# Kernel tuning notes

Measured on AMD Instinct MI355X. Metric: run time of the kernel, lower is better.

## Reference

```python
import jax, jax.numpy as jnp
import numpy as np

N = 100000          # nodes
E = 1600000         # edges (before self-loops)
F_IN = 128          # dataset.num_node_features
HID = 32            # hidden_channels
HEADS = 4
NUM_CLASSES = 40
NEG_SLOPE = 0.2     # PyG GATConv default


def setup_inputs() -> dict:
    key = jax.random.key(0)
    ks = jax.random.split(key, 16)
    x = jax.random.normal(ks[0], (N, F_IN), dtype=jnp.float32)
    edge_index = jax.random.randint(ks[1], (2, E), 0, N, dtype=jnp.int64)

    def glorot(k, shape):
        lim = float(np.sqrt(6.0 / (shape[0] + shape[-1])))
        return jax.random.uniform(k, shape, jnp.float32, -lim, lim)

    # layer 0: F_IN -> HID, heads=HEADS, concat
    W0 = glorot(ks[2], (F_IN, HEADS * HID))
    as0 = glorot(ks[3], (HEADS, HID))
    ad0 = glorot(ks[4], (HEADS, HID))
    b0 = jnp.zeros((HEADS * HID,), jnp.float32)
    # layer 1: HEADS*HID -> HID, heads=HEADS, concat
    W1 = glorot(ks[5], (HEADS * HID, HEADS * HID))
    as1 = glorot(ks[6], (HEADS, HID))
    ad1 = glorot(ks[7], (HEADS, HID))
    b1 = jnp.zeros((HEADS * HID,), jnp.float32)
    # layer 2: HEADS*HID -> HID, heads=1, no concat
    W2 = glorot(ks[8], (HEADS * HID, HID))
    as2 = glorot(ks[9], (1, HID))
    ad2 = glorot(ks[10], (1, HID))
    b2 = jnp.zeros((HID,), jnp.float32)
    # final linear HID -> NUM_CLASSES
    lin_w = glorot(ks[11], (HID, NUM_CLASSES))
    lin_b = jnp.zeros((NUM_CLASSES,), jnp.float32)
    return dict(x=x, edge_index=edge_index, W0=W0, as0=as0, ad0=ad0, b0=b0,
                W1=W1, as1=as1, ad1=ad1, b1=b1,
                W2=W2, as2=as2, ad2=ad2, b2=b2, lin_w=lin_w, lin_b=lin_b)


def gat_conv(x, src, dst, W, a_src, a_dst, b, heads, out_ch, concat):
    n = x.shape[0]
    h = (x @ W).reshape(n, heads, out_ch)               # [N,H,C]
    alpha_s = (h * a_src).sum(-1)                        # [N,H]
    alpha_d = (h * a_dst).sum(-1)                        # [N,H]
    e = jax.nn.leaky_relu(alpha_s[src] + alpha_d[dst], NEG_SLOPE)  # [E,H]
    m = jax.ops.segment_max(e, dst, num_segments=n)      # segment softmax over in-edges
    e = jnp.exp(e - m[dst])
    denom = jax.ops.segment_sum(e, dst, num_segments=n)
    alpha = e / (denom[dst] + 1e-16)                     # [E,H]
    out = jax.ops.segment_sum(h[src] * alpha[:, :, None], dst, num_segments=n)  # [N,H,C]
    out = out.reshape(n, heads * out_ch) if concat else out.mean(axis=1)
    return out + b


def reference(x, edge_index, W0, as0, ad0, b0, W1, as1, ad1, b1,
              W2, as2, ad2, b2, lin_w, lin_b):
    n = x.shape[0]
    loop = jnp.arange(n, dtype=edge_index.dtype)
    src = jnp.concatenate([edge_index[0], loop])   # PyG GATConv adds self-loops
    dst = jnp.concatenate([edge_index[1], loop])
    x = jax.nn.relu(gat_conv(x, src, dst, W0, as0, ad0, b0, HEADS, HID, True))
    x = jax.nn.relu(gat_conv(x, src, dst, W1, as1, ad1, b1, HEADS, HID, True))
    x = jax.nn.relu(gat_conv(x, src, dst, W2, as2, ad2, b2, 1, HID, False))
    return x @ lin_w + lin_b
```

## Files before the change

### kernel.cpp

```cpp
#include <hip/hip_runtime.h>
#include <hip/hip_bf16.h>
#include <hip/hip_fp16.h>
#include <math.h>


#define NEG_SLOPE 0.2f

typedef __attribute__((ext_vector_type(8))) _Float16 f16x8;
typedef __attribute__((ext_vector_type(4))) float    f32x4;


__global__ void zero1_kernel(int* __restrict__ a, int n) {
    int i = blockIdx.x * blockDim.x + threadIdx.x;
    if (i < n) a[i] = 0;
}

__global__ void count_rank_kernel(const int* __restrict__ ei, int eraw, int n,
                                  int* __restrict__ deg, int* __restrict__ rank) {
    int i = blockIdx.x * blockDim.x + threadIdx.x;
    int etot = eraw + n;
    if (i >= etot) return;
    int dst = (i < eraw) ? ei[eraw + i] : (i - eraw);
    rank[i] = atomicAdd(&deg[dst], 1);
}

__global__ __launch_bounds__(1024)
void scan_local_kernel(const int* __restrict__ deg, int* __restrict__ rowptr,
                       int* __restrict__ bsum, int n) {
    __shared__ int buf[1024];
    int tid = threadIdx.x;
    int i = blockIdx.x * 1024 + tid;
    int v = (i < n) ? deg[i] : 0;
    buf[tid] = v;
    __syncthreads();
    for (int off = 1; off < 1024; off <<= 1) {
        int t = (tid >= off) ? buf[tid - off] : 0;
        __syncthreads();
        buf[tid] += t;
        __syncthreads();
    }
    if (i < n) rowptr[i] = buf[tid] - v;
    if (tid == 1023) bsum[blockIdx.x] = buf[1023];
}

__global__ __launch_bounds__(128)
void scan_sums_kernel(const int* __restrict__ bsum, int* __restrict__ boffs, int nb) {
    __shared__ int buf[128];
    int tid = threadIdx.x;
    int v = (tid < nb) ? bsum[tid] : 0;
    buf[tid] = v;
    __syncthreads();
    for (int off = 1; off < 128; off <<= 1) {
        int t = (tid >= off) ? buf[tid - off] : 0;
        __syncthreads();
        buf[tid] += t;
        __syncthreads();
    }
    if (tid < nb) boffs[tid] = buf[tid] - v;
}

__global__ void scan_add_kernel(int* __restrict__ rowptr, const int* __restrict__ boffs,
                                int n, int etot) {
    int i = blockIdx.x * blockDim.x + threadIdx.x;
    if (i < n) rowptr[i] += boffs[i >> 10];
    if (i == 0) rowptr[n] = etot;
}

__global__ void scatter2_kernel(const int* __restrict__ ei, const int* __restrict__ rank,
                                int eraw, int n, const int* __restrict__ rowptr,
                                int* __restrict__ csr_src) {
    int i = blockIdx.x * blockDim.x + threadIdx.x;
    int etot = eraw + n;
    if (i >= etot) return;
    int src, dst;
    if (i < eraw) { src = ei[i]; dst = ei[eraw + i]; }
    else          { src = i - eraw; dst = src; }
    csr_src[rowptr[dst] + rank[i]] = src;
}


__global__ void wt_f16_kernel(const float* __restrict__ W, __half* __restrict__ Wt) {
    int i = blockIdx.x * blockDim.x + threadIdx.x;
    int k = i >> 7, c = i & 127;
    Wt[c * 128 + k] = __float2half(W[i]);
}


__global__ __launch_bounds__(256)
void gemm_mfma_f32in_kernel(const float* __restrict__ X, const __half* __restrict__ Wt,
                            __half* __restrict__ H, int n) {
    int t = threadIdx.x;
    int wave = t >> 6, lane = t & 63;
    int l15 = lane & 15;
    int kg  = lane >> 4;
    int base = blockIdx.x * 64 + wave * 16;
    int row  = base + l15;
    int rowc = (row < n) ? row : 0;

    f32x4 acc[8];
#pragma unroll
    for (int i = 0; i < 8; i++) acc[i] = (f32x4){0.f, 0.f, 0.f, 0.f};

    const float* xp = X + (size_t)rowc * 128 + kg * 8;
#pragma unroll
    for (int ks = 0; ks < 4; ks++) {
        float4 x0 = *(const float4*)(xp + ks * 32);
        float4 x1 = *(const float4*)(xp + ks * 32 + 4);
        f16x8 a;
        a[0] = (_Float16)x0.x; a[1] = (_Float16)x0.y; a[2] = (_Float16)x0.z; a[3] = (_Float16)x0.w;
        a[4] = (_Float16)x1.x; a[5] = (_Float16)x1.y; a[6] = (_Float16)x1.z; a[7] = (_Float16)x1.w;
#pragma unroll
        for (int ct = 0; ct < 8; ct++) {
            f16x8 b = *(const f16x8*)(Wt + (size_t)(ct * 16 + l15) * 128 + ks * 32 + kg * 8);
            acc[ct] = __builtin_amdgcn_mfma_f32_16x16x32_f16(a, b, acc[ct], 0, 0, 0);
        }
    }

#pragma unroll
    for (int ct = 0; ct < 8; ct++) {
#pragma unroll
        for (int r = 0; r < 4; r++) {
            int orow = base + kg * 4 + r;
            if (orow < n)
                H[(size_t)orow * 128 + ct * 16 + l15] = __float2half(acc[ct][r]);
        }
    }
}

__global__ __launch_bounds__(256)
void gemm_mfma_f16in_kernel(const __half* __restrict__ X, const __half* __restrict__ Wt,
                            __half* __restrict__ H, int n) {
    int t = threadIdx.x;
    int wave = t >> 6, lane = t & 63;
    int l15 = lane & 15;
    int kg  = lane >> 4;
    int base = blockIdx.x * 64 + wave * 16;
    int row  = base + l15;
    int rowc = (row < n) ? row : 0;

    f32x4 acc[8];
#pragma unroll
    for (int i = 0; i < 8; i++) acc[i] = (f32x4){0.f, 0.f, 0.f, 0.f};

    const __half* xp = X + (size_t)rowc * 128 + kg * 8;
#pragma unroll
    for (int ks = 0; ks < 4; ks++) {
        f16x8 a = *(const f16x8*)(xp + ks * 32);
#pragma unroll
        for (int ct = 0; ct < 8; ct++) {
            f16x8 b = *(const f16x8*)(Wt + (size_t)(ct * 16 + l15) * 128 + ks * 32 + kg * 8);
            acc[ct] = __builtin_amdgcn_mfma_f32_16x16x32_f16(a, b, acc[ct], 0, 0, 0);
        }
    }

#pragma unroll
    for (int ct = 0; ct < 8; ct++) {
#pragma unroll
        for (int r = 0; r < 4; r++) {
            int orow = base + kg * 4 + r;
            if (orow < n)
                H[(size_t)orow * 128 + ct * 16 + l15] = __float2half(acc[ct][r]);
        }
    }
}


__global__ __launch_bounds__(128)
void gemm_l2_f16_kernel(const __half* __restrict__ X, const float* __restrict__ W,
                        __half* __restrict__ H, int n) {
    __shared__ float xs[8][129];
    int base = blockIdx.x * 8;
    int tid = threadIdx.x;
#pragma unroll
    for (int it = 0; it < 4; it++) {
        int i = tid + it * 128;
        int r = i >> 6, c2 = i & 63;
        int row = base + r;
        __half2 v = (row < n) ? ((const __half2*)(X + (size_t)row * 128))[c2]
                              : __floats2half2_rn(0.f, 0.f);
        float2 f = __half22float2(v);
        xs[r][c2 * 2] = f.x; xs[r][c2 * 2 + 1] = f.y;
    }
    __syncthreads();
    int col  = tid & 31;
    int rsub = tid >> 5;
    float acc0 = 0.f, acc1 = 0.f;
    for (int k = 0; k < 128; k++) {
        float w = W[k * 32 + col];
        acc0 += xs[rsub][k] * w;
        acc1 += xs[rsub + 4][k] * w;
    }
    int row0 = base + rsub;
    if (row0 < n)     H[(size_t)row0 * 32 + col]       = __float2half(acc0);
    if (row0 + 4 < n) H[(size_t)(row0 + 4) * 32 + col] = __float2half(acc1);
}


__global__ void attn_coef_f16_kernel(const __half* __restrict__ H,
                                     const float* __restrict__ a_s,
                                     const float* __restrict__ a_d,
                                     float* __restrict__ as_out,
                                     float* __restrict__ ad_out, int n) {
    int i = blockIdx.x * blockDim.x + threadIdx.x;
    if (i >= n * 4) return;
    int node = i >> 2, h = i & 3;
    const __half2* hp = (const __half2*)(H + (size_t)node * 128 + h * 32);
    float s = 0.f, d = 0.f;
#pragma unroll
    for (int c2 = 0; c2 < 16; c2++) {
        float2 v = __half22float2(hp[c2]);
        s += v.x * a_s[h * 32 + c2 * 2] + v.y * a_s[h * 32 + c2 * 2 + 1];
        d += v.x * a_d[h * 32 + c2 * 2] + v.y * a_d[h * 32 + c2 * 2 + 1];
    }
    as_out[i] = s;
    ad_out[i] = d;
}

__global__ void attn_coef_l2_f16_kernel(const __half* __restrict__ H,
                                        const float* __restrict__ a_s,
                                        const float* __restrict__ a_d,
                                        float* __restrict__ as_out,
                                        float* __restrict__ ad_out, int n) {
    int i = blockIdx.x * blockDim.x + threadIdx.x;
    if (i >= n) return;
    const __half2* hp = (const __half2*)(H + (size_t)i * 32);
    float s = 0.f, d = 0.f;
#pragma unroll
    for (int c2 = 0; c2 < 16; c2++) {
        float2 v = __half22float2(hp[c2]);
        s += v.x * a_s[2 * c2] + v.y * a_s[2 * c2 + 1];
        d += v.x * a_d[2 * c2] + v.y * a_d[2 * c2 + 1];
    }
    as_out[i] = s;
    ad_out[i] = d;
}


struct h4pack { __half2 a, b; };

__global__ __launch_bounds__(256)
void gat_fused_f16_kernel(const __half* __restrict__ Hm,
                          const float* __restrict__ as_,
                          const float* __restrict__ ad_,
                          const int* __restrict__ rowptr,
                          const int* __restrict__ csr,
                          const float* __restrict__ bias,
                          __half* __restrict__ out, int n) {
    constexpr int GS = 32;
    int t = threadIdx.x;
    int node = blockIdx.x * 8 + (t >> 5);
    if (node >= n) return;
    int tl = t & 31;
    int h  = tl >> 3;
    int k8 = tl & 7;
    const uint2* H8 = (const uint2*)Hm;
    int e0 = rowptr[node], e1 = rowptr[node + 1];
    float ad_d = ad_[(size_t)node * 4 + h];

    int  ce  = e0 + k8;
    bool vA  = ce < e1;
    int  idxA = vA ? csr[ce] : 0;
    float asA = vA ? as_[(size_t)idxA * 4 + h] : 0.f;

    float m = -INFINITY, l = 0.f;
    float4 acc = make_float4(0.f, 0.f, 0.f, 0.f);

    for (int eb = e0; eb < e1; eb += 8) {
        uint2 u[8];
#pragma unroll
        for (int j = 0; j < 8; j++) {
            int src = __shfl(idxA, j, 8);
            u[j] = H8[(size_t)src * GS + tl];
        }

        int  ne  = eb + 8 + k8;
        bool vB  = ne < e1;
        int  idxB = vB ? csr[ne] : 0;
        float asB = vB ? as_[(size_t)idxB * 4 + h] : 0.f;

        float el = asA + ad_d;
        el = (el > 0.f) ? el : NEG_SLOPE * el;
        el = vA ? el : -INFINITY;

        float cm = el;
        cm = fmaxf(cm, __shfl_xor(cm, 1, 8));
        cm = fmaxf(cm, __shfl_xor(cm, 2, 8));
        cm = fmaxf(cm, __shfl_xor(cm, 4, 8));
        float m_new = fmaxf(m, cm);
        float scale = __expf(m - m_new);
        float p = vA ? __expf(el - m_new) : 0.f;

        float ps = p;
        ps += __shfl_xor(ps, 1, 8);
        ps += __shfl_xor(ps, 2, 8);
        ps += __shfl_xor(ps, 4, 8);
        l = l * scale + ps;
        acc.x *= scale; acc.y *= scale; acc.z *= scale; acc.w *= scale;
        m = m_new;

#pragma unroll
        for (int j = 0; j < 8; j++) {
            float pj  = __shfl(p, j, 8);
            float2 f01 = __half22float2(*(const __half2*)&u[j].x);
            float2 f23 = __half22float2(*(const __half2*)&u[j].y);
            acc.x += pj * f01.x; acc.y += pj * f01.y;
            acc.z += pj * f23.x; acc.w += pj * f23.y;
        }
        idxA = idxB; asA = asB; vA = vB;
    }

    float li = 1.f / (l + 1e-16f);
    float4 b4 = ((const float4*)bias)[tl];
    float4 o;
    o.x = fmaxf(acc.x * li + b4.x, 0.f);
    o.y = fmaxf(acc.y * li + b4.y, 0.f);
    o.z = fmaxf(acc.z * li + b4.z, 0.f);
    o.w = fmaxf(acc.w * li + b4.w, 0.f);
    h4pack po;
    po.a = __floats2half2_rn(o.x, o.y);
    po.b = __floats2half2_rn(o.z, o.w);
    ((h4pack*)out)[(size_t)node * 32 + tl] = po;
}


__global__ __launch_bounds__(256)
void gat_fused_l2_kernel(const __half* __restrict__ Hm,
                         const float* __restrict__ as_,
                         const float* __restrict__ ad_,
                         const int* __restrict__ rowptr,
                         const int* __restrict__ csr,
                         const float* __restrict__ bias,
                         const float* __restrict__ lw,
                         const float* __restrict__ lb,
                         float* __restrict__ out, int n) {
    int t = threadIdx.x;
    int node = blockIdx.x * 32 + (t >> 3);
    if (node >= n) return;
    int tl = t & 7;
    const uint2* H8 = (const uint2*)Hm;
    int e0 = rowptr[node], e1 = rowptr[node + 1];
    float ad_d = ad_[node];

    int  ce  = e0 + tl;
    bool vA  = ce < e1;
    int  idxA = vA ? csr[ce] : 0;
    float asA = vA ? as_[idxA] : 0.f;

    float m = -INFINITY, l = 0.f;
    float4 acc = make_float4(0.f, 0.f, 0.f, 0.f);

    for (int eb = e0; eb < e1; eb += 8) {
        uint2 u[8];
#pragma unroll
        for (int j = 0; j < 8; j++) {
            int src = __shfl(idxA, j, 8);
            u[j] = H8[(size_t)src * 8 + tl];
        }

        int  ne  = eb + 8 + tl;
        bool vB  = ne < e1;
        int  idxB = vB ? csr[ne] : 0;
        float asB = vB ? as_[idxB] : 0.f;

        float el = asA + ad_d;
        el = (el > 0.f) ? el : NEG_SLOPE * el;
        el = vA ? el : -INFINITY;

        float cm = el;
        cm = fmaxf(cm, __shfl_xor(cm, 1, 8));
        cm = fmaxf(cm, __shfl_xor(cm, 2, 8));
        cm = fmaxf(cm, __shfl_xor(cm, 4, 8));
        float m_new = fmaxf(m, cm);
        float scale = __expf(m - m_new);
        float p = vA ? __expf(el - m_new) : 0.f;

        float ps = p;
        ps += __shfl_xor(ps, 1, 8);
        ps += __shfl_xor(ps, 2, 8);
        ps += __shfl_xor(ps, 4, 8);
        l = l * scale + ps;
        acc.x *= scale; acc.y *= scale; acc.z *= scale; acc.w *= scale;
        m = m_new;

#pragma unroll
        for (int j = 0; j < 8; j++) {
            float pj  = __shfl(p, j, 8);
            float2 f01 = __half22float2(*(const __half2*)&u[j].x);
            float2 f23 = __half22float2(*(const __half2*)&u[j].y);
            acc.x += pj * f01.x; acc.y += pj * f01.y;
            acc.z += pj * f23.x; acc.w += pj * f23.y;
        }
        idxA = idxB; asA = asB; vA = vB;
    }

    float li = 1.f / (l + 1e-16f);
    float4 b4 = ((const float4*)bias)[tl];
    float4 o;
    o.x = fmaxf(acc.x * li + b4.x, 0.f);
    o.y = fmaxf(acc.y * li + b4.y, 0.f);
    o.z = fmaxf(acc.z * li + b4.z, 0.f);
    o.w = fmaxf(acc.w * li + b4.w, 0.f);

    float fin0 = lb[tl];
    float fin1 = lb[tl + 8];
    float fin2 = lb[tl + 16];
    float fin3 = lb[tl + 24];
    float fin4 = lb[tl + 32];
#pragma unroll
    for (int j = 0; j < 8; j++) {
        float vx = __shfl(o.x, j, 8);
        float vy = __shfl(o.y, j, 8);
        float vz = __shfl(o.z, j, 8);
        float vw = __shfl(o.w, j, 8);
        const float* l0 = lw + (size_t)(4 * j) * 40;
#pragma unroll
        for (int c = 0; c < 5; c++) {
            int cls = tl + 8 * c;
            float v = vx * l0[cls] + vy * l0[40 + cls] + vz * l0[80 + cls] + vw * l0[120 + cls];
            if (c == 0) fin0 += v;
            else if (c == 1) fin1 += v;
            else if (c == 2) fin2 += v;
            else if (c == 3) fin3 += v;
            else fin4 += v;
        }
    }
    float* op = out + (size_t)node * 40;
    op[tl]      = fin0;
    op[tl + 8]  = fin1;
    op[tl + 16] = fin2;
    op[tl + 24] = fin3;
    op[tl + 32] = fin4;
}


extern "C" void kernel_launch(void* const* d_in, const int* in_sizes, int n_in,
                              void* d_out, int out_size, void* d_ws, size_t ws_size,
                              hipStream_t stream) {
    const float* x   = (const float*)d_in[0];
    const int*   ei  = (const int*)d_in[1];
    const float* W0  = (const float*)d_in[2];
    const float* as0 = (const float*)d_in[3];
    const float* ad0 = (const float*)d_in[4];
    const float* b0  = (const float*)d_in[5];
    const float* W1  = (const float*)d_in[6];
    const float* as1 = (const float*)d_in[7];
    const float* ad1 = (const float*)d_in[8];
    const float* b1  = (const float*)d_in[9];
    const float* W2  = (const float*)d_in[10];
    const float* as2 = (const float*)d_in[11];
    const float* ad2 = (const float*)d_in[12];
    const float* b2  = (const float*)d_in[13];
    const float* lw  = (const float*)d_in[14];
    const float* lb  = (const float*)d_in[15];
    float* out = (float*)d_out;

    const int n    = in_sizes[0] / 128;
    const int eraw = in_sizes[1] / 2;
    const int etot = eraw + n;
    const int nb   = (n + 1023) / 1024;

    char* wsp = (char*)d_ws;
    size_t off = 0;
    auto alloc = [&](size_t bytes) -> void* {
        void* p = wsp + off;
        off += (bytes + 255) & ~(size_t)255;
        return p;
    };
    __half* h16    = (__half*)alloc((size_t)n * 128 * 2);
    __half* buf16  = (__half*)alloc((size_t)n * 128 * 2);
    __half* h2     = (__half*)alloc((size_t)n * 32 * 2);
    __half* Wt0    = (__half*)alloc((size_t)128 * 128 * 2);
    __half* Wt1    = (__half*)alloc((size_t)128 * 128 * 2);
    float*  asb    = (float*)alloc((size_t)n * 4 * 4);
    float*  adb    = (float*)alloc((size_t)n * 4 * 4);
    int*    deg    = (int*)alloc((size_t)n * 4);
    int*    rank   = (int*)alloc((size_t)etot * 4);
    int*    rowptr = (int*)alloc((size_t)(n + 1) * 4);
    int*    csr    = (int*)alloc((size_t)etot * 4);
    int*    bsum   = (int*)alloc((size_t)nb * 4);
    int*    boffs  = (int*)alloc((size_t)nb * 4);

    zero1_kernel<<<(n + 255) / 256, 256, 0, stream>>>(deg, n);
    count_rank_kernel<<<(etot + 255) / 256, 256, 0, stream>>>(ei, eraw, n, deg, rank);
    wt_f16_kernel<<<64, 256, 0, stream>>>(W0, Wt0);
    wt_f16_kernel<<<64, 256, 0, stream>>>(W1, Wt1);
    scan_local_kernel<<<nb, 1024, 0, stream>>>(deg, rowptr, bsum, n);
    scan_sums_kernel<<<1, 128, 0, stream>>>(bsum, boffs, nb);
    scan_add_kernel<<<(n + 255) / 256, 256, 0, stream>>>(rowptr, boffs, n, etot);
    scatter2_kernel<<<(etot + 255) / 256, 256, 0, stream>>>(ei, rank, eraw, n, rowptr, csr);

    gemm_mfma_f32in_kernel<<<(n + 63) / 64, 256, 0, stream>>>(x, Wt0, h16, n);
    attn_coef_f16_kernel<<<(n * 4 + 255) / 256, 256, 0, stream>>>(h16, as0, ad0, asb, adb, n);
    gat_fused_f16_kernel<<<(n + 7) / 8, 256, 0, stream>>>(h16, asb, adb, rowptr, csr, b0, buf16, n);

    gemm_mfma_f16in_kernel<<<(n + 63) / 64, 256, 0, stream>>>(buf16, Wt1, h16, n);
    attn_coef_f16_kernel<<<(n * 4 + 255) / 256, 256, 0, stream>>>(h16, as1, ad1, asb, adb, n);
    gat_fused_f16_kernel<<<(n + 7) / 8, 256, 0, stream>>>(h16, asb, adb, rowptr, csr, b1, buf16, n);

    gemm_l2_f16_kernel<<<(n + 7) / 8, 128, 0, stream>>>(buf16, W2, h2, n);
    attn_coef_l2_f16_kernel<<<(n + 255) / 256, 256, 0, stream>>>(h2, as2, ad2, asb, adb, n);
    gat_fused_l2_kernel<<<(n + 31) / 32, 256, 0, stream>>>(h2, asb, adb, rowptr, csr, b2, lw, lb, out, n);
}
```

Baseline: 528.8 us.

## Fuse attention coefficients into MFMA GEMM epilogue with packed weights and 2 row tiles

Attention-coefficient dot products for layers 0 and 1 now run in the GEMM epilogue from the fp32 accumulators, reduced with 16-lane shuffles. This removes two separate coefficient kernels and their re-read of the fp16 H. Weights are pre-packed into the MFMA lane order so each B fragment is a contiguous load. Each wave now computes two 16-row tiles that share each B load, so there are half as many blocks and more registers per thread. The coefficients also change slightly because they are computed from the fp32 accumulators rather than the rounded fp16 values.

After: 501.1 us. -5.2%, faster.

```diff
diff --git a/kernel.cpp b/kernel.cpp
--- a/kernel.cpp
+++ b/kernel.cpp
@@ -79,87 +79,104 @@
 }
 
 
-__global__ void wt_f16_kernel(const float* __restrict__ W, __half* __restrict__ Wt) {
-    int i = blockIdx.x * blockDim.x + threadIdx.x;
-    int k = i >> 7, c = i & 127;
-    Wt[c * 128 + k] = __float2half(W[i]);
-}
-
-
+__global__ void wpack_f16_kernel(const float* __restrict__ W, __half* __restrict__ Wp) {
+    int i = blockIdx.x * blockDim.x + threadIdx.x;
+    int j    = i & 7;
+    int lane = (i >> 3) & 63;
+    int ks   = (i >> 9) & 3;
+    int ct   = i >> 11;
+    int k = ks * 32 + (lane >> 4) * 8 + j;
+    int c = ct * 16 + (lane & 15);
+    Wp[i] = __float2half(W[k * 128 + c]);
+}
+
+
+template <bool F32IN>
 __global__ __launch_bounds__(256)
-void gemm_mfma_f32in_kernel(const float* __restrict__ X, const __half* __restrict__ Wt,
-                            __half* __restrict__ H, int n) {
+void gemm_mfma_coef_kernel(const void* __restrict__ Xv, const __half* __restrict__ Wp,
+                           const float* __restrict__ a_s, const float* __restrict__ a_d,
+                           __half* __restrict__ H, float* __restrict__ as_out,
+                           float* __restrict__ ad_out, int n) {
     int t = threadIdx.x;
     int wave = t >> 6, lane = t & 63;
     int l15 = lane & 15;
     int kg  = lane >> 4;
-    int base = blockIdx.x * 64 + wave * 16;
-    int row  = base + l15;
-    int rowc = (row < n) ? row : 0;
-
-    f32x4 acc[8];
-#pragma unroll
-    for (int i = 0; i < 8; i++) acc[i] = (f32x4){0.f, 0.f, 0.f, 0.f};
-
-    const float* xp = X + (size_t)rowc * 128 + kg * 8;
+    int base = blockIdx.x * 128 + wave * 32;
+
+    int row0 = base + l15;
+    int row1 = base + 16 + l15;
+    int r0c = (row0 < n) ? row0 : 0;
+    int r1c = (row1 < n) ? row1 : 0;
+
+    f32x4 acc[2][8];
+#pragma unroll
+    for (int tt = 0; tt < 2; tt++)
+#pragma unroll
+        for (int i = 0; i < 8; i++) acc[tt][i] = (f32x4){0.f, 0.f, 0.f, 0.f};
+
 #pragma unroll
     for (int ks = 0; ks < 4; ks++) {
-        float4 x0 = *(const float4*)(xp + ks * 32);
-        float4 x1 = *(const float4*)(xp + ks * 32 + 4);
-        f16x8 a;
-        a[0] = (_Float16)x0.x; a[1] = (_Float16)x0.y; a[2] = (_Float16)x0.z; a[3] = (_Float16)x0.w;
-        a[4] = (_Float16)x1.x; a[5] = (_Float16)x1.y; a[6] = (_Float16)x1.z; a[7] = (_Float16)x1.w;
+        f16x8 a0, a1;
+        if constexpr (F32IN) {
+            const float* X = (const float*)Xv;
+            const float* p0 = X + (size_t)r0c * 128 + kg * 8 + ks * 32;
+            const float* p1 = X + (size_t)r1c * 128 + kg * 8 + ks * 32;
+            float4 x0 = *(const float4*)(p0), x1 = *(const float4*)(p0 + 4);
+            a0[0] = (_Float16)x0.x; a0[1] = (_Float16)x0.y; a0[2] = (_Float16)x0.z; a0[3] = (_Float16)x0.w;
+            a0[4] = (_Float16)x1.x; a0[5] = (_Float16)x1.y; a0[6] = (_Float16)x1.z; a0[7] = (_Float16)x1.w;
+            float4 y0 = *(const float4*)(p1), y1 = *(const float4*)(p1 + 4);
+            a1[0] = (_Float16)y0.x; a1[1] = (_Float16)y0.y; a1[2] = (_Float16)y0.z; a1[3] = (_Float16)y0.w;
+            a1[4] = (_Float16)y1.x; a1[5] = (_Float16)y1.y; a1[6] = (_Float16)y1.z; a1[7] = (_Float16)y1.w;
+        } else {
+            const __half* X = (const __half*)Xv;
+            a0 = *(const f16x8*)(X + (size_t)r0c * 128 + kg * 8 + ks * 32);
+            a1 = *(const f16x8*)(X + (size_t)r1c * 128 + kg * 8 + ks * 32);
+        }
 #pragma unroll
         for (int ct = 0; ct < 8; ct++) {
-            f16x8 b = *(const f16x8*)(Wt + (size_t)(ct * 16 + l15) * 128 + ks * 32 + kg * 8);
-            acc[ct] = __builtin_amdgcn_mfma_f32_16x16x32_f16(a, b, acc[ct], 0, 0, 0);
-        }
-    }
-
-#pragma unroll
-    for (int ct = 0; ct < 8; ct++) {
-#pragma unroll
-        for (int r = 0; r < 4; r++) {
-            int orow = base + kg * 4 + r;
-            if (orow < n)
-                H[(size_t)orow * 128 + ct * 16 + l15] = __float2half(acc[ct][r]);
-        }
-    }
-}
-
-__global__ __launch_bounds__(256)
-void gemm_mfma_f16in_kernel(const __half* __restrict__ X, const __half* __restrict__ Wt,
-                            __half* __restrict__ H, int n) {
-    int t = threadIdx.x;
-    int wave = t >> 6, lane = t & 63;
-    int l15 = lane & 15;
-    int kg  = lane >> 4;
-    int base = blockIdx.x * 64 + wave * 16;
-    int row  = base + l15;
-    int rowc = (row < n) ? row : 0;
-
-    f32x4 acc[8];
-#pragma unroll
-    for (int i = 0; i < 8; i++) acc[i] = (f32x4){0.f, 0.f, 0.f, 0.f};
-
-    const __half* xp = X + (size_t)rowc * 128 + kg * 8;
-#pragma unroll
-    for (int ks = 0; ks < 4; ks++) {
-        f16x8 a = *(const f16x8*)(xp + ks * 32);
+            f16x8 b = *(const f16x8*)(Wp + (size_t)((ct * 4 + ks) * 64 + lane) * 8);
+            acc[0][ct] = __builtin_amdgcn_mfma_f32_16x16x32_f16(a0, b, acc[0][ct], 0, 0, 0);
+            acc[1][ct] = __builtin_amdgcn_mfma_f32_16x16x32_f16(a1, b, acc[1][ct], 0, 0, 0);
+        }
+    }
+
+#pragma unroll
+    for (int tt = 0; tt < 2; tt++) {
 #pragma unroll
         for (int ct = 0; ct < 8; ct++) {
-            f16x8 b = *(const f16x8*)(Wt + (size_t)(ct * 16 + l15) * 128 + ks * 32 + kg * 8);
-            acc[ct] = __builtin_amdgcn_mfma_f32_16x16x32_f16(a, b, acc[ct], 0, 0, 0);
-        }
-    }
-
-#pragma unroll
-    for (int ct = 0; ct < 8; ct++) {
-#pragma unroll
-        for (int r = 0; r < 4; r++) {
-            int orow = base + kg * 4 + r;
-            if (orow < n)
-                H[(size_t)orow * 128 + ct * 16 + l15] = __float2half(acc[ct][r]);
+#pragma unroll
+            for (int r = 0; r < 4; r++) {
+                int orow = base + tt * 16 + kg * 4 + r;
+                if (orow < n)
+                    H[(size_t)orow * 128 + ct * 16 + l15] = __float2half(acc[tt][ct][r]);
+            }
+        }
+    }
+
+#pragma unroll
+    for (int h = 0; h < 4; h++) {
+        float ws0 = a_s[h * 32 + l15];
+        float ws1 = a_s[h * 32 + 16 + l15];
+        float wd0 = a_d[h * 32 + l15];
+        float wd1 = a_d[h * 32 + 16 + l15];
+#pragma unroll
+        for (int tt = 0; tt < 2; tt++) {
+#pragma unroll
+            for (int r = 0; r < 4; r++) {
+                float v0 = acc[tt][2 * h][r];
+                float v1 = acc[tt][2 * h + 1][r];
+                float ps = v0 * ws0 + v1 * ws1;
+                float pd = v0 * wd0 + v1 * wd1;
+                ps += __shfl_xor(ps, 1, 16); pd += __shfl_xor(pd, 1, 16);
+                ps += __shfl_xor(ps, 2, 16); pd += __shfl_xor(pd, 2, 16);
+                ps += __shfl_xor(ps, 4, 16); pd += __shfl_xor(pd, 4, 16);
+                ps += __shfl_xor(ps, 8, 16); pd += __shfl_xor(pd, 8, 16);
+                int orow = base + tt * 16 + kg * 4 + r;
+                if (l15 == 0 && orow < n) {
+                    as_out[(size_t)orow * 4 + h] = ps;
+                    ad_out[(size_t)orow * 4 + h] = pd;
+                }
+            }
         }
     }
 }
@@ -193,27 +210,6 @@
     int row0 = base + rsub;
     if (row0 < n)     H[(size_t)row0 * 32 + col]       = __float2half(acc0);
     if (row0 + 4 < n) H[(size_t)(row0 + 4) * 32 + col] = __float2half(acc1);
-}
-
-
-__global__ void attn_coef_f16_kernel(const __half* __restrict__ H,
-                                     const float* __restrict__ a_s,
-                                     const float* __restrict__ a_d,
-                                     float* __restrict__ as_out,
-                                     float* __restrict__ ad_out, int n) {
-    int i = blockIdx.x * blockDim.x + threadIdx.x;
-    if (i >= n * 4) return;
-    int node = i >> 2, h = i & 3;
-    const __half2* hp = (const __half2*)(H + (size_t)node * 128 + h * 32);
-    float s = 0.f, d = 0.f;
-#pragma unroll
-    for (int c2 = 0; c2 < 16; c2++) {
-        float2 v = __half22float2(hp[c2]);
-        s += v.x * a_s[h * 32 + c2 * 2] + v.y * a_s[h * 32 + c2 * 2 + 1];
-        d += v.x * a_d[h * 32 + c2 * 2] + v.y * a_d[h * 32 + c2 * 2 + 1];
-    }
-    as_out[i] = s;
-    ad_out[i] = d;
 }
 
 __global__ void attn_coef_l2_f16_kernel(const __half* __restrict__ H,
@@ -469,8 +465,8 @@
     __half* h16    = (__half*)alloc((size_t)n * 128 * 2);
     __half* buf16  = (__half*)alloc((size_t)n * 128 * 2);
     __half* h2     = (__half*)alloc((size_t)n * 32 * 2);
-    __half* Wt0    = (__half*)alloc((size_t)128 * 128 * 2);
-    __half* Wt1    = (__half*)alloc((size_t)128 * 128 * 2);
+    __half* Wp0    = (__half*)alloc((size_t)128 * 128 * 2);
+    __half* Wp1    = (__half*)alloc((size_t)128 * 128 * 2);
     float*  asb    = (float*)alloc((size_t)n * 4 * 4);
     float*  adb    = (float*)alloc((size_t)n * 4 * 4);
     int*    deg    = (int*)alloc((size_t)n * 4);
@@ -482,19 +478,19 @@
 
     zero1_kernel<<<(n + 255) / 256, 256, 0, stream>>>(deg, n);
     count_rank_kernel<<<(etot + 255) / 256, 256, 0, stream>>>(ei, eraw, n, deg, rank);
-    wt_f16_kernel<<<64, 256, 0, stream>>>(W0, Wt0);
-    wt_f16_kernel<<<64, 256, 0, stream>>>(W1, Wt1);
+    wpack_f16_kernel<<<64, 256, 0, stream>>>(W0, Wp0);
+    wpack_f16_kernel<<<64, 256, 0, stream>>>(W1, Wp1);
     scan_local_kernel<<<nb, 1024, 0, stream>>>(deg, rowptr, bsum, n);
     scan_sums_kernel<<<1, 128, 0, stream>>>(bsum, boffs, nb);
     scan_add_kernel<<<(n + 255) / 256, 256, 0, stream>>>(rowptr, boffs, n, etot);
     scatter2_kernel<<<(etot + 255) / 256, 256, 0, stream>>>(ei, rank, eraw, n, rowptr, csr);
 
-    gemm_mfma_f32in_kernel<<<(n + 63) / 64, 256, 0, stream>>>(x, Wt0, h16, n);
-    attn_coef_f16_kernel<<<(n * 4 + 255) / 256, 256, 0, stream>>>(h16, as0, ad0, asb, adb, n);
+    const int gblocks = (n + 127) / 128;
+
+    gemm_mfma_coef_kernel<true><<<gblocks, 256, 0, stream>>>(x, Wp0, as0, ad0, h16, asb, adb, n);
     gat_fused_f16_kernel<<<(n + 7) / 8, 256, 0, stream>>>(h16, asb, adb, rowptr, csr, b0, buf16, n);
 
-    gemm_mfma_f16in_kernel<<<(n + 63) / 64, 256, 0, stream>>>(buf16, Wt1, h16, n);
-    attn_coef_f16_kernel<<<(n * 4 + 255) / 256, 256, 0, stream>>>(h16, as1, ad1, asb, adb, n);
+    gemm_mfma_coef_kernel<false><<<gblocks, 256, 0, stream>>>(buf16, Wp1, as1, ad1, h16, asb, adb, n);
     gat_fused_f16_kernel<<<(n + 7) / 8, 256, 0, stream>>>(h16, asb, adb, rowptr, csr, b1, buf16, n);
 
     gemm_l2_f16_kernel<<<(n + 7) / 8, 128, 0, stream>>>(buf16, W2, h2, n);
```
